# Optimization experiments

Hardware: AMD Instinct MI355X
Metric: run time of the kernel (lower is better)

## Reference

```python
import jax, jax.numpy as jnp
import numpy as np
from jax import lax

NEG = -1.0e30  # finite stand-in for -inf (keeps vjp NaN-free)


def _ctc_losses(log_probs, input_lengths, targets, target_lengths, blank=0):
    """Per-sequence CTC negative log-likelihood (Graves 2006 forward algorithm).

    log_probs: (B,T,V) log-softmax outputs; targets: (B,U) padded labels (no blanks).
    Matches torch.nn.functional.ctc_loss(..., reduction='none') semantics per sequence.
    """
    B, T, V = log_probs.shape
    U = targets.shape[1]
    S = 2 * U + 1
    s = jnp.arange(S)
    tgt_idx = jnp.clip((s - 1) // 2, 0, U - 1)
    # Blank-interleaved extended label sequence: b, y1, b, y2, ..., yU, b
    ext = jnp.where((s % 2) == 0, blank, targets[:, tgt_idx])  # (B,S)
    ext_m2 = jnp.concatenate([jnp.full((B, 2), blank, ext.dtype), ext[:, :-2]], axis=1)
    can_skip = (ext != blank) & (ext != ext_m2) & (s >= 2)[None, :]
    idx = jnp.broadcast_to(ext[:, None, :], (B, T, S))
    lp_ext = jnp.take_along_axis(log_probs, idx, axis=2)  # (B,T,S)

    alpha0 = jnp.full((B, S), NEG, log_probs.dtype)
    alpha0 = alpha0.at[:, 0].set(lp_ext[:, 0, 0]).at[:, 1].set(lp_ext[:, 0, 1])
    neg1 = jnp.full((B, 1), NEG, log_probs.dtype)
    neg2 = jnp.full((B, 2), NEG, log_probs.dtype)

    def step(alpha, inp):
        lp_t, t = inp
        a1 = jnp.concatenate([neg1, alpha[:, :-1]], axis=1)
        a2 = jnp.concatenate([neg2, alpha[:, :-2]], axis=1)
        a2 = jnp.where(can_skip, a2, NEG)
        new = jnp.logaddexp(jnp.logaddexp(alpha, a1), a2) + lp_t
        # freeze alpha once past this sequence's input length
        alpha = jnp.where((t < input_lengths)[:, None], new, alpha)
        return alpha, None

    lp_seq = jnp.transpose(lp_ext[:, 1:, :], (1, 0, 2))  # (T-1,B,S)
    alpha, _ = lax.scan(step, alpha0, (lp_seq, jnp.arange(1, T)))
    end = 2 * target_lengths  # index of final blank in extended sequence
    a_blank = jnp.take_along_axis(alpha, end[:, None], axis=1)[:, 0]
    a_label = jnp.take_along_axis(alpha, jnp.maximum(end - 1, 0)[:, None], axis=1)[:, 0]
    return -jnp.logaddexp(a_blank, a_label)  # (B,)


def setup_inputs() -> dict:
    key = jax.random.key(0)
    k1, k2, k3, k4, k5, k6 = jax.random.split(key, 6)
    N, T, C, V, U = 16, 1000, 512, 2000, 100
    # Two augmented views of the same N utterances, stacked along batch (cr-ctc)
    enc_half = jax.random.normal(k1, (N, T, C), dtype=jnp.float32)
    encoder_out = jnp.concatenate(
        [enc_half, enc_half + 0.1 * jax.random.normal(k2, (N, T, C), dtype=jnp.float32)], axis=0)
    lens_half = jax.random.randint(k3, (N,), T // 2, T + 1, dtype=jnp.int32)
    encoder_out_lens = jnp.concatenate([lens_half, lens_half])
    tgt_half = jax.random.randint(k4, (N, U), 1, V, dtype=jnp.int32)  # labels in [1,V), 0 = blank
    targets = jnp.concatenate([tgt_half, tgt_half], axis=0)
    tl_half = jax.random.randint(k5, (N,), U // 2, U + 1, dtype=jnp.int32)
    target_lengths = jnp.concatenate([tl_half, tl_half])
    W = jax.random.normal(k6, (V, C), dtype=jnp.float32) * np.float32(1.0 / np.sqrt(C))
    b = jnp.zeros((V,), dtype=jnp.float32)
    return {"encoder_out": encoder_out, "W": W, "b": b,
            "encoder_out_lens": encoder_out_lens, "targets": targets,
            "target_lengths": target_lengths}


def reference(encoder_out, W, b, encoder_out_lens, targets, target_lengths):
    # ctc_output head: (Dropout is identity in eval) Linear -> LogSoftmax
    B, T, C = encoder_out.shape
    logits = jnp.einsum('btc,vc->btv', encoder_out, W) + b
    log_probs = jax.nn.log_softmax(logits, axis=-1)  # (B,T,V)
    # CTC loss, reduction='sum'
    ctc_loss = jnp.sum(_ctc_losses(log_probs, encoder_out_lens, targets, target_lengths))
    # Consistency regularization: KL(input=log p || target=log q), log_target=True,
    # q = detached log-probs of the swapped batch halves
    half = B // 2
    q = lax.stop_gradient(jnp.concatenate([log_probs[half:], log_probs[:half]], axis=0))
    kl = jnp.exp(q) * (q - log_probs)
    pad = (jnp.arange(T)[None, :] >= encoder_out_lens[:, None])[:, :, None]  # make_pad_mask
    cr_loss = jnp.sum(jnp.where(pad, 0.0, kl))
    return (0.5 * ctc_loss, 0.5 * cr_loss)
```

## Files before the change

kernel.cpp:

```cpp
#include <hip/hip_runtime.h>
#include <hip/hip_bf16.h>
#include <cstdint>

#define NEG (-1.0e30f)
#define INVLN2 1.44269504088896340736f
#define LN2    0.69314718055994530942f

typedef unsigned short u16;
typedef __attribute__((ext_vector_type(8))) short short8;
typedef __attribute__((ext_vector_type(4))) float f32x4;

typedef const __attribute__((address_space(1))) void cg_void;
typedef __attribute__((address_space(3))) void lds_void;

#define Bsz   32
#define Tlen  1000
#define Cdim  512
#define Vdim  2000
#define Udim  100
#define Mrows (Bsz * Tlen)
#define Npad  2048
#define GROW  256

#define WS_ABF 0u
#define WS_G   0u
#define WS_WBF 32768000u
#define WS_KL  WS_WBF
#define WS_Z   (WS_WBF + 2097152u)
#define WS_ACC (WS_Z + 128000000u)

__device__ inline u16 f2bf(float x) {
  uint32_t u = __float_as_uint(x);
  uint32_t r = (u + 0x7fffu + ((u >> 16) & 1u)) >> 16;
  return (u16)r;
}
__device__ inline float bf2f(u16 u) {
  return __uint_as_float(((uint32_t)u) << 16);
}

#define DPP_MAX_STAGE(m, ctrl) { \
    int _r = __builtin_amdgcn_update_dpp(__float_as_int(m), __float_as_int(m), \
                                         ctrl, 0xF, 0xF, false); \
    m = fmaxf(m, __int_as_float(_r)); }
#define DPP_SUM_STAGE(v, ctrl) { \
    int _r = __builtin_amdgcn_update_dpp(0, __float_as_int(v), \
                                         ctrl, 0xF, 0xF, true); \
    v += __int_as_float(_r); }

__device__ inline float dppMax64(float m) {
  DPP_MAX_STAGE(m, 0x111) DPP_MAX_STAGE(m, 0x112) DPP_MAX_STAGE(m, 0x114)
  DPP_MAX_STAGE(m, 0x118) DPP_MAX_STAGE(m, 0x142) DPP_MAX_STAGE(m, 0x143)
  return m;
}
__device__ inline float dppSum64(float v) {
  DPP_SUM_STAGE(v, 0x111) DPP_SUM_STAGE(v, 0x112) DPP_SUM_STAGE(v, 0x114)
  DPP_SUM_STAGE(v, 0x118) DPP_SUM_STAGE(v, 0x142) DPP_SUM_STAGE(v, 0x143)
  return v;
}

__device__ inline float shiftup1(float x, float fill) {
  int r = __builtin_amdgcn_update_dpp(__float_as_int(fill), __float_as_int(x),
                                      0x138, 0xF, 0xF, false);
  return __int_as_float(r);
}

__global__ void convert_kernel(const float4* __restrict__ enc4, const float4* __restrict__ W4,
                               uint4* __restrict__ a4, uint4* __restrict__ w4,
                               const int* __restrict__ lens,
                               float* __restrict__ accum) {
  int idx = blockIdx.x * blockDim.x + threadIdx.x;
  int stride = gridDim.x * blockDim.x;
  if (idx == 0) { accum[0] = 0.0f; accum[1] = 0.0f; }
  const int nA = Mrows * Cdim / 8;
  const int nW = Vdim * Cdim / 8;
  const int nWp = Npad * Cdim / 8;
  for (int i = idx; i < nA; i += stride) {
    int row = i >> 6;
    int b = row / 1000;
    int t = row - b * 1000;
    if (t >= lens[b]) continue;
    float4 x = enc4[2 * i], y = enc4[2 * i + 1];
    uint4 o;
    o.x = (uint32_t)f2bf(x.x) | ((uint32_t)f2bf(x.y) << 16);
    o.y = (uint32_t)f2bf(x.z) | ((uint32_t)f2bf(x.w) << 16);
    o.z = (uint32_t)f2bf(y.x) | ((uint32_t)f2bf(y.y) << 16);
    o.w = (uint32_t)f2bf(y.z) | ((uint32_t)f2bf(y.w) << 16);
    a4[i] = o;
  }
  for (int i = idx; i < nWp; i += stride) {
    uint4 o = {0, 0, 0, 0};
    if (i < nW) {
      float4 x = W4[2 * i], y = W4[2 * i + 1];
      o.x = (uint32_t)f2bf(x.x) | ((uint32_t)f2bf(x.y) << 16);
      o.y = (uint32_t)f2bf(x.z) | ((uint32_t)f2bf(x.w) << 16);
      o.z = (uint32_t)f2bf(y.x) | ((uint32_t)f2bf(y.y) << 16);
      o.w = (uint32_t)f2bf(y.z) | ((uint32_t)f2bf(y.w) << 16);
    }
    w4[i] = o;
  }
}

__global__ __launch_bounds__(256) void gemm_kernel(const u16* __restrict__ A,
                                                   const u16* __restrict__ Wb,
                                                   const int* __restrict__ lens,
                                                   u16* __restrict__ Z) {
  const int id = blockIdx.x;
  const int c = id >> 7, r = id & 127;
  int mTile, nTile;
  if (c < 31) { mTile = c * 8 + (r & 7); nTile = r >> 3; }
  else        { mTile = 248 + (r & 1);   nTile = r >> 1; }
  const int mBase = mTile * 128;
  const int nBase = nTile * 128;
  {
    int bSeq = mBase / 1000;
    int t0 = mBase - bSeq * 1000;
    if (t0 <= 872 && t0 >= lens[bSeq]) return;
  }

  __shared__ __attribute__((aligned(16))) u16 As[2][128 * 64];
  __shared__ __attribute__((aligned(16))) u16 Bs[2][128 * 64];
  const int tid = threadIdx.x;
  const int wave = tid >> 6;
  const int lane = tid & 63;
  const int m_lane = lane & 15;
  const int quad = lane >> 4;

  auto STAGE = [&](int k0, int s) {
    #pragma unroll
    for (int rr = 0; rr < 4; ++rr) {
      int u = rr * 256 + tid;
      int g = u >> 3;
      int q = (u & 7) ^ (g & 7);
      const u16* gpA = A + ((size_t)(mBase + g) << 9) + (k0 + (q << 3));
      __builtin_amdgcn_global_load_lds((cg_void*)gpA, (lds_void*)&As[s][(rr * 4 + wave) * 512],
                                       16, 0, 0);
      const u16* gpB = Wb + ((size_t)(nBase + g) << 9) + (k0 + (q << 3));
      __builtin_amdgcn_global_load_lds((cg_void*)gpB, (lds_void*)&Bs[s][(rr * 4 + wave) * 512],
                                       16, 0, 0);
    }
  };

  f32x4 acc[4][4];
  const f32x4 zero4 = {0.0f, 0.0f, 0.0f, 0.0f};
  #pragma unroll
  for (int i = 0; i < 4; ++i)
    #pragma unroll
    for (int j = 0; j < 4; ++j) acc[i][j] = zero4;

  STAGE(0, 0);
  __syncthreads();

  #pragma unroll
  for (int t = 0; t < 8; ++t) {
    const int s = t & 1;
    if (t < 7) STAGE((t + 1) * 64, s ^ 1);
    #pragma unroll
    for (int kk = 0; kk < 2; ++kk) {
      short8 af[4], bfv[4];
      #pragma unroll
      for (int mi = 0; mi < 4; ++mi) {
        int row = (wave >> 1) * 64 + mi * 16 + m_lane;
        int q = (kk * 4 + quad) ^ (row & 7);
        af[mi] = *(const short8*)&As[s][row * 64 + (q << 3)];
      }
      #pragma unroll
      for (int ni = 0; ni < 4; ++ni) {
        int col = (wave & 1) * 64 + ni * 16 + m_lane;
        int q = (kk * 4 + quad) ^ (col & 7);
        bfv[ni] = *(const short8*)&Bs[s][col * 64 + (q << 3)];
      }
      __builtin_amdgcn_s_setprio(1);
      #pragma unroll
      for (int mi = 0; mi < 4; ++mi)
        #pragma unroll
        for (int ni = 0; ni < 4; ++ni)
          acc[mi][ni] = __builtin_amdgcn_mfma_f32_16x16x32_bf16(af[mi], bfv[ni],
                                                                acc[mi][ni], 0, 0, 0);
      __builtin_amdgcn_s_setprio(0);
    }
    if (t < 7) __syncthreads();
  }

  #pragma unroll
  for (int ni = 0; ni < 4; ++ni) {
    int col = nBase + (wave & 1) * 64 + ni * 16 + m_lane;
    if (col < Vdim) {
      #pragma unroll
      for (int mi = 0; mi < 4; ++mi) {
        int row0 = mBase + (wave >> 1) * 64 + mi * 16 + quad * 4;
        #pragma unroll
        for (int rg = 0; rg < 4; ++rg)
          Z[(size_t)(row0 + rg) * Vdim + col] = f2bf(acc[mi][ni][rg]);
      }
    }
  }
}

__global__ __launch_bounds__(256) void cr_stats_kernel(const u16* __restrict__ Z,
                                                       const float* __restrict__ bias,
                                                       const int* __restrict__ lens,
                                                       const int* __restrict__ targets,
                                                       const int* __restrict__ tlens,
                                                       float* __restrict__ G,
                                                       float* __restrict__ klp) {
  int bp = blockIdx.x;
  int t = blockIdx.y;
  int tid = threadIdx.x;
  size_t r1 = (size_t)bp * Tlen + t;
  if (t >= lens[bp]) {
    if (tid == 0) klp[r1] = 0.0f;
    return;
  }
  int wave = tid >> 6, lane = tid & 63;
  size_t r2 = r1 + (size_t)16 * Tlen;
  const u16* z1 = Z + r1 * Vdim;
  const u16* z2 = Z + r2 * Vdim;

  __shared__ __attribute__((aligned(16))) float ls1[Vdim];
  __shared__ __attribute__((aligned(16))) float ls2[Vdim];
  __shared__ float red[8];

  const int c0 = tid * 8;
  float v1[8], v2[8], e1[8], e2[8];
  float mx1 = NEG, mx2 = NEG;
  if (c0 < Vdim) {
    short8 za = *(const short8*)&z1[c0];
    short8 zb = *(const short8*)&z2[c0];
    float4 b0 = *(const float4*)&bias[c0];
    float4 b1 = *(const float4*)&bias[c0 + 4];
    float bb[8] = {b0.x, b0.y, b0.z, b0.w, b1.x, b1.y, b1.z, b1.w};
    #pragma unroll
    for (int j = 0; j < 8; ++j) {
      v1[j] = bf2f((u16)za[j]) + bb[j];
      v2[j] = bf2f((u16)zb[j]) + bb[j];
      mx1 = fmaxf(mx1, v1[j]);
      mx2 = fmaxf(mx2, v2[j]);
    }
    *(float4*)&ls1[c0]     = (float4){v1[0], v1[1], v1[2], v1[3]};
    *(float4*)&ls1[c0 + 4] = (float4){v1[4], v1[5], v1[6], v1[7]};
    *(float4*)&ls2[c0]     = (float4){v2[0], v2[1], v2[2], v2[3]};
    *(float4*)&ls2[c0 + 4] = (float4){v2[4], v2[5], v2[6], v2[7]};
  } else {
    #pragma unroll
    for (int j = 0; j < 8; ++j) { v1[j] = NEG; v2[j] = NEG; }
  }
  float w1 = dppMax64(mx1), w2 = dppMax64(mx2);
  if (lane == 63) { red[wave] = w1; red[4 + wave] = w2; }
  __syncthreads();
  float M1 = fmaxf(fmaxf(red[0], red[1]), fmaxf(red[2], red[3]));
  float M2 = fmaxf(fmaxf(red[4], red[5]), fmaxf(red[6], red[7]));
  __syncthreads();
  float s1 = 0.0f, s2 = 0.0f;
  #pragma unroll
  for (int j = 0; j < 8; ++j) {
    e1[j] = expf(v1[j] - M1);
    e2[j] = expf(v2[j] - M2);
    s1 += e1[j];
    s2 += e2[j];
  }
  s1 = dppSum64(s1); s2 = dppSum64(s2);
  if (lane == 63) { red[wave] = s1; red[4 + wave] = s2; }
  __syncthreads();
  float S1 = red[0] + red[1] + red[2] + red[3];
  float S2 = red[4] + red[5] + red[6] + red[7];
  float c1 = M1 + logf(S1);
  float c2 = M2 + logf(S2);
  float inv1 = 1.0f / S1;
  float inv2 = 1.0f / S2;

  if (tid < 64) {
    int i1 = min(2 * tid, Udim - 1);
    int i3 = min(2 * tid + 1, Udim - 1);
    int t1a = targets[bp * Udim + i1];
    int t1b = targets[bp * Udim + i3];
    int t2a = targets[(bp + 16) * Udim + i1];
    int t2b = targets[(bp + 16) * Udim + i3];
    int tl1 = tlens[bp];
    int tl2 = tlens[bp + 16];
    float4 g1 = {(2 * tid < tl1) ? expf(ls1[t1a] - c1) : 0.0f,
                 (2 * tid + 1 < tl1) ? expf(ls1[t1b] - c1) : 0.0f,
                 expf(ls1[0] - c1), 0.0f};
    float4 g2 = {(2 * tid < tl2) ? expf(ls2[t2a] - c2) : 0.0f,
                 (2 * tid + 1 < tl2) ? expf(ls2[t2b] - c2) : 0.0f,
                 expf(ls2[0] - c2), 0.0f};
    *(float4*)(G + r1 * GROW + 4 * tid) = g1;
    *(float4*)(G + r2 * GROW + 4 * tid) = g2;
  }

  float f = 0.0f;
  #pragma unroll
  for (int j = 0; j < 8; ++j) {
    float p1 = e1[j] * inv1;
    float p2 = e2[j] * inv2;
    f += (p1 - p2) * (v1[j] - v2[j]);
  }
  __syncthreads();
  f = dppSum64(f);
  if (lane == 63) red[wave] = f;
  __syncthreads();
  if (tid == 0) {
    klp[r1] = red[0] + red[1] + red[2] + red[3];
  }
}

#define DECL3(p, i) float p##i##x, p##i##y, p##i##b;
#define LOADR(p, i, row) { float4 v = *(const float4*)(gb + (size_t)(row) * GROW + 4 * lane); \
    p##i##x = v.x; p##i##y = v.y; p##i##b = v.z; }

#define COMPU(p, i) { \
    float pX = p##i##x, pY = p##i##y, pB = p##i##b; \
    float p3 = shiftup1(a3, 0.0f); \
    float t01 = a1 + a0; \
    float t23 = a3 + a2; \
    float n0 = (a0 + p3) * pB; \
    float n1 = fmaf(p3, fm1, t01) * pX; \
    float n2 = (a2 + a1) * pB; \
    float n3 = fmaf(a1, fm3, t23) * pY; \
    a0 = n0; a1 = n1; a2 = n2; a3 = n3; }

#define COMPA(p, i, off) { \
    float pX = p##i##x, pY = p##i##y, pB = p##i##b; \
    float p3 = shiftup1(a3, 0.0f); \
    float t01 = a1 + a0; \
    float t23 = a3 + a2; \
    float n0 = (a0 + p3) * pB; \
    float n1 = fmaf(p3, fm1, t01) * pX; \
    float n2 = (a2 + a1) * pB; \
    float n3 = fmaf(a1, fm3, t23) * pY; \
    bool act = (t + (off)) < len; \
    a0 = act ? n0 : a0; a1 = act ? n1 : a1; \
    a2 = act ? n2 : a2; a3 = act ? n3 : a3; }

#define DPPMAX(m, ctrl) { int _r = __builtin_amdgcn_update_dpp(0,              \
      __float_as_int(m), ctrl, 0xF, 0xF, true);                               \
    m = fmaxf(m, __int_as_float(_r)); }

#define RESCALE_KILL(tdone) {                                                 \
    int R = len - 1 - (tdone); R = R < 0 ? 0 : R;                             \
    int lo = end1 - 2 * R;                                                    \
    a0 = (base4 + 0 >= lo) ? a0 : 0.0f;                                       \
    a1 = (base4 + 1 >= lo) ? a1 : 0.0f;                                       \
    a2 = (base4 + 2 >= lo) ? a2 : 0.0f;                                       \
    a3 = (base4 + 3 >= lo) ? a3 : 0.0f;                                       \
    float m = fmaxf(fmaxf(a0, a1), fmaxf(a2, a3));                            \
    DPPMAX(m, 0x111) DPPMAX(m, 0x112) DPPMAX(m, 0x114) DPPMAX(m, 0x118)       \
    DPPMAX(m, 0x142) DPPMAX(m, 0x143)                                         \
    uint32_t mb = (uint32_t)__builtin_amdgcn_readlane(__float_as_int(m), 63); \
    int e = (int)((mb >> 23) & 0xffu);                                        \
    int sh = 227 - e;                                                         \
    sh = sh > 127 ? 127 : (sh < -126 ? -126 : sh);                            \
    float sc = __uint_as_float((uint32_t)(sh + 127) << 23);                   \
    a0 *= sc; a1 *= sc; a2 *= sc; a3 *= sc;                                   \
    logScale -= sh; }

#define LOAD32(p, base) \
    LOADR(p, 0,  (base) + 0)  LOADR(p, 1,  (base) + 1)  LOADR(p, 2,  (base) + 2)  LOADR(p, 3,  (base) + 3)  \
    LOADR(p, 4,  (base) + 4)  LOADR(p, 5,  (base) + 5)  LOADR(p, 6,  (base) + 6)  LOADR(p, 7,  (base) + 7)  \
    LOADR(p, 8,  (base) + 8)  LOADR(p, 9,  (base) + 9)  LOADR(p, 10, (base) + 10) LOADR(p, 11, (base) + 11) \
    LOADR(p, 12, (base) + 12) LOADR(p, 13, (base) + 13) LOADR(p, 14, (base) + 14) LOADR(p, 15, (base) + 15) \
    LOADR(p, 16, (base) + 16) LOADR(p, 17, (base) + 17) LOADR(p, 18, (base) + 18) LOADR(p, 19, (base) + 19) \
    LOADR(p, 20, (base) + 20) LOADR(p, 21, (base) + 21) LOADR(p, 22, (base) + 22) LOADR(p, 23, (base) + 23) \
    LOADR(p, 24, (base) + 24) LOADR(p, 25, (base) + 25) LOADR(p, 26, (base) + 26) LOADR(p, 27, (base) + 27) \
    LOADR(p, 28, (base) + 28) LOADR(p, 29, (base) + 29) LOADR(p, 30, (base) + 30) LOADR(p, 31, (base) + 31)

#define COMPU32(p, tb) \
    COMPU(p, 0)  COMPU(p, 1)  COMPU(p, 2)  COMPU(p, 3)  \
    COMPU(p, 4)  COMPU(p, 5)  COMPU(p, 6)  COMPU(p, 7)  \
    RESCALE_KILL((tb) + 7) \
    COMPU(p, 8)  COMPU(p, 9)  COMPU(p, 10) COMPU(p, 11) \
    COMPU(p, 12) COMPU(p, 13) COMPU(p, 14) COMPU(p, 15) \
    RESCALE_KILL((tb) + 15) \
    COMPU(p, 16) COMPU(p, 17) COMPU(p, 18) COMPU(p, 19) \
    COMPU(p, 20) COMPU(p, 21) COMPU(p, 22) COMPU(p, 23) \
    RESCALE_KILL((tb) + 23) \
    COMPU(p, 24) COMPU(p, 25) COMPU(p, 26) COMPU(p, 27) \
    COMPU(p, 28) COMPU(p, 29) COMPU(p, 30) COMPU(p, 31) \
    RESCALE_KILL((tb) + 31)

#define COMPA32(p, o) \
    COMPA(p, 0,  (o) + 0)  COMPA(p, 1,  (o) + 1)  COMPA(p, 2,  (o) + 2)  COMPA(p, 3,  (o) + 3)  \
    COMPA(p, 4,  (o) + 4)  COMPA(p, 5,  (o) + 5)  COMPA(p, 6,  (o) + 6)  COMPA(p, 7,  (o) + 7)  \
    RESCALE_KILL(t + (o) + 7) \
    COMPA(p, 8,  (o) + 8)  COMPA(p, 9,  (o) + 9)  COMPA(p, 10, (o) + 10) COMPA(p, 11, (o) + 11) \
    COMPA(p, 12, (o) + 12) COMPA(p, 13, (o) + 13) COMPA(p, 14, (o) + 14) COMPA(p, 15, (o) + 15) \
    RESCALE_KILL(t + (o) + 15) \
    COMPA(p, 16, (o) + 16) COMPA(p, 17, (o) + 17) COMPA(p, 18, (o) + 18) COMPA(p, 19, (o) + 19) \
    COMPA(p, 20, (o) + 20) COMPA(p, 21, (o) + 21) COMPA(p, 22, (o) + 22) COMPA(p, 23, (o) + 23) \
    RESCALE_KILL(t + (o) + 23) \
    COMPA(p, 24, (o) + 24) COMPA(p, 25, (o) + 25) COMPA(p, 26, (o) + 26) COMPA(p, 27, (o) + 27) \
    COMPA(p, 28, (o) + 28) COMPA(p, 29, (o) + 29) COMPA(p, 30, (o) + 30) COMPA(p, 31, (o) + 31) \
    RESCALE_KILL(t + (o) + 31)

#define DECL32(p) \
    DECL3(p, 0)  DECL3(p, 1)  DECL3(p, 2)  DECL3(p, 3)  DECL3(p, 4)  DECL3(p, 5)  DECL3(p, 6)  DECL3(p, 7)  \
    DECL3(p, 8)  DECL3(p, 9)  DECL3(p, 10) DECL3(p, 11) DECL3(p, 12) DECL3(p, 13) DECL3(p, 14) DECL3(p, 15) \
    DECL3(p, 16) DECL3(p, 17) DECL3(p, 18) DECL3(p, 19) DECL3(p, 20) DECL3(p, 21) DECL3(p, 22) DECL3(p, 23) \
    DECL3(p, 24) DECL3(p, 25) DECL3(p, 26) DECL3(p, 27) DECL3(p, 28) DECL3(p, 29) DECL3(p, 30) DECL3(p, 31)

__global__ __launch_bounds__(64, 1) void ctc_kernel(const float* __restrict__ G,
                                                    const int* __restrict__ targets,
                                                    const int* __restrict__ lens,
                                                    const int* __restrict__ tlens,
                                                    float* __restrict__ accum) {
  int b = blockIdx.x;
  int lane = threadIdx.x;
  const int* tgt = targets + b * Udim;
  int i1 = min(2 * lane, Udim - 1);
  int i3 = min(2 * lane + 1, Udim - 1);
  int l1 = tgt[i1];
  int l3 = tgt[i3];
  int lm1 = tgt[min(max(2 * lane - 1, 0), Udim - 1)];
  const float fm1 = ((lane >= 1) && (l1 != lm1)) ? 1.0f : 0.0f;
  const float fm3 = (l3 != l1) ? 1.0f : 0.0f;
  int len = lens[b];
  int tl = tlens[b];
  const int end1 = 2 * tl - 1;
  const int base4 = 4 * lane;
  const float* gb = G + (size_t)b * Tlen * GROW;

  float4 v0 = *(const float4*)(gb + 4 * lane);
  float a0 = (lane == 0) ? v0.z : 0.0f;
  float a1 = (lane == 0) ? v0.x : 0.0f;
  float a2 = 0.0f, a3 = 0.0f;
  int logScale = 0;

  DECL32(sA)
  DECL32(sB)

  LOAD32(sA, 1)

  int steps = len - 1;
  int mainN = steps & ~63;
  int t = 1;
  for (int blk = 0; blk < mainN; blk += 64) {
    LOAD32(sB, t + 32)
    __builtin_amdgcn_sched_barrier(0);
    COMPU32(sA, t)
    LOAD32(sA, t + 64)
    __builtin_amdgcn_sched_barrier(0);
    COMPU32(sB, t + 32)
    t += 64;
  }
  {
    LOAD32(sB, t + 32)
    __builtin_amdgcn_sched_barrier(0);
    COMPA32(sA, 0)
    COMPA32(sB, 32)
  }

  __shared__ float fin[256];
  fin[4 * lane + 0] = a0;
  fin[4 * lane + 1] = a1;
  fin[4 * lane + 2] = a2;
  fin[4 * lane + 3] = a3;
  __syncthreads();
  if (lane == 0) {
    int end = 2 * tl;
    float sum = fin[end] + fin[end - 1];
    float loss = -LN2 * (log2f(sum) + (float)logScale);
    atomicAdd(&accum[0], 0.5f * loss);
  }
}

__global__ __launch_bounds__(1024) void finalize_kernel(const float* __restrict__ accum,
                                                        const float* __restrict__ klp,
                                                        float* __restrict__ out) {
  __shared__ float red[16];
  int tid = threadIdx.x;
  float s = 0.0f;
  for (int i = tid; i < 16 * Tlen; i += 1024) s += klp[i];
  s = dppSum64(s);
  int wave = tid >> 6, lane = tid & 63;
  if (lane == 63) red[wave] = s;
  __syncthreads();
  if (tid == 0) {
    float tot = 0.0f;
    #pragma unroll
    for (int w = 0; w < 16; ++w) tot += red[w];
    out[0] = accum[0];
    out[1] = 0.5f * tot;
  }
}

extern "C" void kernel_launch(void* const* d_in, const int* in_sizes, int n_in,
                              void* d_out, int out_size, void* d_ws, size_t ws_size,
                              hipStream_t stream) {
  const float* enc = (const float*)d_in[0];
  const float* W = (const float*)d_in[1];
  const float* bias = (const float*)d_in[2];
  const int* lens = (const int*)d_in[3];
  const int* targets = (const int*)d_in[4];
  const int* tlens = (const int*)d_in[5];

  char* ws = (char*)d_ws;
  u16* a_bf = (u16*)(ws + WS_ABF);
  u16* w_bf = (u16*)(ws + WS_WBF);
  u16* Zb   = (u16*)(ws + WS_Z);
  float* Gp  = (float*)(ws + WS_G);
  float* klp = (float*)(ws + WS_KL);
  float* accum = (float*)(ws + WS_ACC);

  hipLaunchKernelGGL(convert_kernel, dim3(1024), dim3(256), 0, stream,
                     (const float4*)enc, (const float4*)W, (uint4*)a_bf, (uint4*)w_bf,
                     lens, accum);
  hipLaunchKernelGGL(gemm_kernel, dim3(4000), dim3(256), 0, stream,
                     a_bf, w_bf, lens, Zb);
  hipLaunchKernelGGL(cr_stats_kernel, dim3(16, 1000), dim3(256), 0, stream,
                     Zb, bias, lens, targets, tlens, Gp, klp);
  hipLaunchKernelGGL(ctc_kernel, dim3(Bsz), dim3(64), 0, stream,
                     Gp, targets, lens, tlens, accum);
  hipLaunchKernelGGL(finalize_kernel, dim3(1), dim3(1024), 0, stream,
                     accum, klp, (float*)d_out);
}
```

Before: 283.6 us.

## Load GEMM MFMA fragments directly from global memory, dropping LDS staging

The logits GEMM no longer stages A and W tiles through double-buffered shared memory with global_load_lds and barriers. Each wave now reads its MFMA operand fragments straight from global memory, relying on L1/L2 caching for reuse across waves. This removes LDS traffic, the swizzle arithmetic and block-wide synchronisation. In exchange it adds redundant global and cache traffic, since waves sharing rows or columns each fetch them separately, and it loses the explicit prefetch overlap.

```diff
diff --git a/kernel.cpp b/kernel.cpp
--- a/kernel.cpp
+++ b/kernel.cpp
@@ -117,28 +117,14 @@
     if (t0 <= 872 && t0 >= lens[bSeq]) return;
   }
 
-  __shared__ __attribute__((aligned(16))) u16 As[2][128 * 64];
-  __shared__ __attribute__((aligned(16))) u16 Bs[2][128 * 64];
   const int tid = threadIdx.x;
   const int wave = tid >> 6;
   const int lane = tid & 63;
   const int m_lane = lane & 15;
   const int quad = lane >> 4;
 
-  auto STAGE = [&](int k0, int s) {
-    #pragma unroll
-    for (int rr = 0; rr < 4; ++rr) {
-      int u = rr * 256 + tid;
-      int g = u >> 3;
-      int q = (u & 7) ^ (g & 7);
-      const u16* gpA = A + ((size_t)(mBase + g) << 9) + (k0 + (q << 3));
-      __builtin_amdgcn_global_load_lds((cg_void*)gpA, (lds_void*)&As[s][(rr * 4 + wave) * 512],
-                                       16, 0, 0);
-      const u16* gpB = Wb + ((size_t)(nBase + g) << 9) + (k0 + (q << 3));
-      __builtin_amdgcn_global_load_lds((cg_void*)gpB, (lds_void*)&Bs[s][(rr * 4 + wave) * 512],
-                                       16, 0, 0);
-    }
-  };
+  const u16* Ap = A + ((size_t)(mBase + (wave >> 1) * 64 + m_lane) << 9) + quad * 8;
+  const u16* Bp = Wb + ((size_t)(nBase + (wave & 1) * 64 + m_lane) << 9) + quad * 8;
 
   f32x4 acc[4][4];
   const f32x4 zero4 = {0.0f, 0.0f, 0.0f, 0.0f};
@@ -147,38 +133,23 @@
     #pragma unroll
     for (int j = 0; j < 4; ++j) acc[i][j] = zero4;
 
-  STAGE(0, 0);
-  __syncthreads();
-
   #pragma unroll
-  for (int t = 0; t < 8; ++t) {
-    const int s = t & 1;
-    if (t < 7) STAGE((t + 1) * 64, s ^ 1);
-    #pragma unroll
-    for (int kk = 0; kk < 2; ++kk) {
-      short8 af[4], bfv[4];
+  for (int kc = 0; kc < 16; ++kc) {
+    short8 af[4], bfv[4];
+    #pragma unroll
+    for (int mi = 0; mi < 4; ++mi)
+      af[mi] = *(const short8*)(Ap + (size_t)mi * 16 * 512 + kc * 32);
+    #pragma unroll
+    for (int ni = 0; ni < 4; ++ni)
+      bfv[ni] = *(const short8*)(Bp + (size_t)ni * 16 * 512 + kc * 32);
+    __builtin_amdgcn_s_setprio(1);
+    #pragma unroll
+    for (int mi = 0; mi < 4; ++mi)
       #pragma unroll
-      for (int mi = 0; mi < 4; ++mi) {
-        int row = (wave >> 1) * 64 + mi * 16 + m_lane;
-        int q = (kk * 4 + quad) ^ (row & 7);
-        af[mi] = *(const short8*)&As[s][row * 64 + (q << 3)];
-      }
-      #pragma unroll
-      for (int ni = 0; ni < 4; ++ni) {
-        int col = (wave & 1) * 64 + ni * 16 + m_lane;
-        int q = (kk * 4 + quad) ^ (col & 7);
-        bfv[ni] = *(const short8*)&Bs[s][col * 64 + (q << 3)];
-      }
-      __builtin_amdgcn_s_setprio(1);
-      #pragma unroll
-      for (int mi = 0; mi < 4; ++mi)
-        #pragma unroll
-        for (int ni = 0; ni < 4; ++ni)
-          acc[mi][ni] = __builtin_amdgcn_mfma_f32_16x16x32_bf16(af[mi], bfv[ni],
-                                                                acc[mi][ni], 0, 0, 0);
-      __builtin_amdgcn_s_setprio(0);
-    }
-    if (t < 7) __syncthreads();
+      for (int ni = 0; ni < 4; ++ni)
+        acc[mi][ni] = __builtin_amdgcn_mfma_f32_16x16x32_bf16(af[mi], bfv[ni],
+                                                              acc[mi][ni], 0, 0, 0);
+    __builtin_amdgcn_s_setprio(0);
   }
 
   #pragma unroll
```

After: 442.6 us. 56.1% more time.
